# Kernel tuning notes

Measured on AMD Instinct MI355X. Metric: run time of the kernel, lower is better.

## Reference

```python
import jax, jax.numpy as jnp
import numpy as np

NUM_HEADS = 16


def setup_inputs() -> dict:
    key = jax.random.key(0)
    k1, k2, k3 = jax.random.split(key, 3)
    B, N, C = 8, 1024, 1024
    x = jax.random.normal(k1, (B, N, C), dtype=jnp.float32)
    w_qkv = jax.random.normal(k2, (3 * C, C), dtype=jnp.float32) * (C ** -0.5)
    w_proj = jax.random.normal(k3, (C, C), dtype=jnp.float32) * (C ** -0.5)
    b_proj = jnp.zeros((C,), dtype=jnp.float32)
    return {"x": x, "w_qkv": w_qkv, "w_proj": w_proj, "b_proj": b_proj}


def reference(x, w_qkv, w_proj, b_proj):
    B, N, C = x.shape
    H = NUM_HEADS
    d = C // H
    scale = d ** -0.5
    # qkv projection: (B, N, 3C) -> (3, B, H, N, d)
    qkv = jnp.einsum('bnc,oc->bno', x, w_qkv)
    qkv = qkv.reshape(B, N, 3, H, d).transpose(2, 0, 3, 1, 4)
    q, k, v = qkv[0], qkv[1], qkv[2]
    # spatial attention
    attn = jnp.einsum('bhnd,bhmd->bhnm', q, k) * scale
    attn = jax.nn.softmax(attn, axis=-1)
    out = jnp.einsum('bhnm,bhmd->bhnd', attn, v)
    out = out.transpose(0, 2, 1, 3).reshape(B, N, C)
    # output projection
    return jnp.einsum('bnc,oc->bno', out, w_proj) + b_proj
```

## Files before the change

kernel.cpp:

```cpp
#include <hip/hip_runtime.h>
#include <hip/hip_bf16.h>

typedef unsigned short u16;
typedef unsigned int u32;
typedef __bf16 bf16x8 __attribute__((ext_vector_type(8)));
typedef float f32x4 __attribute__((ext_vector_type(4)));

__device__ __forceinline__ u16 f2b(float f) {
    __bf16 h = (__bf16)f;
    return __builtin_bit_cast(u16, h);
}
__device__ __forceinline__ f32x4 mfma16(bf16x8 a, bf16x8 b, f32x4 c) {
    return __builtin_amdgcn_mfma_f32_16x16x32_bf16(a, b, c, 0, 0, 0);
}
__device__ __forceinline__ void async16(const u16* gsrc, u16* ldst) {
    __builtin_amdgcn_global_load_lds(
        (const __attribute__((address_space(1))) void*)gsrc,
        (__attribute__((address_space(3))) void*)ldst, 16, 0, 0);
}

__global__ __launch_bounds__(256) void cvt_f32_bf16(const float* __restrict__ in,
                                                    u16* __restrict__ out, int n) {
    int i = (blockIdx.x * 256 + threadIdx.x) * 4;
    if (i >= n) return;
    float4 f = *(const float4*)(in + i);
    ushort4 o;
    o.x = f2b(f.x); o.y = f2b(f.y); o.z = f2b(f.z); o.w = f2b(f.w);
    *(ushort4*)(out + i) = o;
}

template <bool F32OUT>
__global__ __launch_bounds__(256) void gemm_bt(const u16* __restrict__ A,
                                               const u16* __restrict__ B,
                                               void* __restrict__ Cptr,
                                               const float* __restrict__ bias,
                                               int N, int K) {
    __shared__ u16 As[128 * 32];
    __shared__ u16 Bs[128 * 32];
    const int tid  = threadIdx.x;
    const int lane = tid & 63, wid = tid >> 6;
    const int quad = lane >> 4, l16 = lane & 15;
    const int bm = blockIdx.y, bn = blockIdx.x;
    const int wm = (wid >> 1) * 64, wn = (wid & 1) * 64;
    const int srow = tid >> 2;
    const int scol = (tid & 3) * 8;

    const u16* Abase = A + (size_t)(bm * 128) * K + scol;
    const u16* Bbase = B + (size_t)(bn * 128) * K + scol;

    f32x4 acc[4][4] = {};

    for (int k0 = 0; k0 < K; k0 += 32) {
        __syncthreads();
        async16(Abase + (size_t)srow * K + k0,        &As[wid * 512]);
        async16(Abase + (size_t)(64 + srow) * K + k0, &As[2048 + wid * 512]);
        async16(Bbase + (size_t)srow * K + k0,        &Bs[wid * 512]);
        async16(Bbase + (size_t)(64 + srow) * K + k0, &Bs[2048 + wid * 512]);
        __syncthreads();
        bf16x8 af[4], bfr[4];
#pragma unroll
        for (int mt = 0; mt < 4; mt++)
            af[mt] = *(const bf16x8*)&As[(wm + mt * 16 + l16) * 32 + quad * 8];
#pragma unroll
        for (int nt = 0; nt < 4; nt++)
            bfr[nt] = *(const bf16x8*)&Bs[(wn + nt * 16 + l16) * 32 + quad * 8];
#pragma unroll
        for (int mt = 0; mt < 4; mt++)
#pragma unroll
            for (int nt = 0; nt < 4; nt++)
                acc[mt][nt] = mfma16(af[mt], bfr[nt], acc[mt][nt]);
    }
#pragma unroll
    for (int mt = 0; mt < 4; mt++) {
#pragma unroll
        for (int nt = 0; nt < 4; nt++) {
            int row = bm * 128 + wm + mt * 16 + quad * 4;
            int col = bn * 128 + wn + nt * 16 + l16;
            float bv = F32OUT ? bias[col] : 0.f;
#pragma unroll
            for (int r = 0; r < 4; r++) {
                if (F32OUT)
                    ((float*)Cptr)[(size_t)(row + r) * N + col] = acc[mt][nt][r] + bv;
                else
                    ((u16*)Cptr)[(size_t)(row + r) * N + col] = f2b(acc[mt][nt][r]);
            }
        }
    }
}

__global__ __launch_bounds__(256, 4) void attn_kernel(const u16* __restrict__ qk,
                                                      const u16* __restrict__ vT,
                                                      u16* __restrict__ outb) {
    __shared__ u16 Qs[64 * 64];
    __shared__ u16 Ks[64 * 64];
    __shared__ u16 Vt[64 * 64];
    __shared__ u16 Ps[4 * 16 * 72];
    const int tid = threadIdx.x, lane = tid & 63, wid = tid >> 6;
    const int quad = lane >> 4, l16 = lane & 15;
    const int qt = blockIdx.x;
    const int bh = blockIdx.y;
    const int b = bh >> 4, h = bh & 15;
    const size_t base = (size_t)b * 1024;
    const int hoff = h * 64;
    const float CEXP = 0.125f * 1.44269504f;

    const int sr_ = lane >> 3;
    const int sc_ = ((lane & 7) ^ sr_) * 8;
    const int sw = l16 & 7;

#pragma unroll
    for (int j = 0; j < 2; ++j) {
        int rg = wid * 16 + j * 8;
        async16(qk + (base + qt * 64 + rg + sr_) * 2048 + hoff + sc_, &Qs[rg * 64]);
    }

    f32x4 Oacc[4] = {};
    float l_i[4] = {0.f, 0.f, 0.f, 0.f};
    bf16x8 aq[2];
    u16* Pw = &Ps[wid * (16 * 72)];

    for (int kt = 0; kt < 16; ++kt) {
        __syncthreads();
#pragma unroll
        for (int j = 0; j < 2; ++j) {
            int rg = wid * 16 + j * 8;
            async16(qk + (base + kt * 64 + rg + sr_) * 2048 + 1024 + hoff + sc_,
                    &Ks[rg * 64]);
            async16(vT + (size_t)(hoff + rg + sr_) * 8192 + base + kt * 64 + sc_,
                    &Vt[rg * 64]);
        }
        __syncthreads();

        if (kt == 0) {
            int row = wid * 16 + l16;
            aq[0] = *(const bf16x8*)&Qs[row * 64 + ((quad ^ sw) << 3)];
            aq[1] = *(const bf16x8*)&Qs[row * 64 + (((4 + quad) ^ sw) << 3)];
        }

        f32x4 sacc[4] = {};
#pragma unroll
        for (int nt = 0; nt < 4; nt++) {
            int row = nt * 16 + l16;
            bf16x8 bk0 = *(const bf16x8*)&Ks[row * 64 + ((quad ^ sw) << 3)];
            bf16x8 bk1 = *(const bf16x8*)&Ks[row * 64 + (((4 + quad) ^ sw) << 3)];
            sacc[nt] = mfma16(aq[0], bk0, sacc[nt]);
            sacc[nt] = mfma16(aq[1], bk1, sacc[nt]);
        }

#pragma unroll
        for (int nt = 0; nt < 4; nt++)
#pragma unroll
            for (int r = 0; r < 4; r++) {
                float p = exp2f(sacc[nt][r] * CEXP);
                l_i[r] += p;
                Pw[(quad * 4 + r) * 72 + nt * 16 + l16] = f2b(p);
            }

        asm volatile("s_waitcnt lgkmcnt(0)" ::: "memory");
        __builtin_amdgcn_wave_barrier();

#pragma unroll
        for (int kc = 0; kc < 2; kc++) {
            bf16x8 ap = *(const bf16x8*)&Pw[l16 * 72 + kc * 32 + quad * 8];
#pragma unroll
            for (int nv = 0; nv < 4; nv++) {
                int row = nv * 16 + l16;
                bf16x8 bv = *(const bf16x8*)&Vt[row * 64 + (((kc * 4 + quad) ^ sw) << 3)];
                Oacc[nv] = mfma16(ap, bv, Oacc[nv]);
            }
        }
    }

#pragma unroll
    for (int off = 1; off < 16; off <<= 1)
#pragma unroll
        for (int r = 0; r < 4; r++) l_i[r] += __shfl_xor(l_i[r], off);

    float inv[4];
#pragma unroll
    for (int r = 0; r < 4; r++) inv[r] = 1.f / l_i[r];
#pragma unroll
    for (int nv = 0; nv < 4; nv++)
#pragma unroll
        for (int r = 0; r < 4; r++) {
            int row = qt * 64 + wid * 16 + quad * 4 + r;
            int col = hoff + nv * 16 + l16;
            outb[(base + row) * 1024 + col] = f2b(Oacc[nv][r] * inv[r]);
        }
}

extern "C" void kernel_launch(void* const* d_in, const int* in_sizes, int n_in,
                              void* d_out, int out_size, void* d_ws, size_t ws_size,
                              hipStream_t stream) {
    const float* x      = (const float*)d_in[0];
    const float* w_qkv  = (const float*)d_in[1];
    const float* w_proj = (const float*)d_in[2];
    const float* b_proj = (const float*)d_in[3];

    char* ws = (char*)d_ws;
    u16* xb     = (u16*)(ws);
    u16* wqkvb  = (u16*)(ws + 16777216);
    u16* wprojb = (u16*)(ws + 23068672);
    u16* qkb    = (u16*)(ws + 25165824);
    u16* vTb    = (u16*)(ws + 58720256);
    u16* attnb  = (u16*)(ws + 75497472);

    cvt_f32_bf16<<<8192, 256, 0, stream>>>(x, xb, 8388608);
    cvt_f32_bf16<<<3072, 256, 0, stream>>>(w_qkv, wqkvb, 3145728);
    cvt_f32_bf16<<<1024, 256, 0, stream>>>(w_proj, wprojb, 1048576);

    gemm_bt<false><<<dim3(16, 64), 256, 0, stream>>>(xb, wqkvb, qkb, nullptr, 2048, 1024);
    gemm_bt<false><<<dim3(64, 8), 256, 0, stream>>>(wqkvb + (size_t)2048 * 1024, xb, vTb,
                                                    nullptr, 8192, 1024);
    attn_kernel<<<dim3(16, 128), 256, 0, stream>>>(qkb, vTb, attnb);
    gemm_bt<true><<<dim3(8, 64), 256, 0, stream>>>(attnb, wprojb, d_out, b_proj, 1024, 1024);
}
```

Baseline: 283.3 us.

## Merge conversion and QKV GEMM launches, transpose score MFMA for packed P stores

The three f32-to-bf16 conversion kernels become one launch that picks its source by index, and the QK and V-transposed GEMMs become a single 1536-block launch sharing a common device routine. This removes launch gaps and the tail of each small grid. In the attention kernel the QK^T MFMA swaps its operands so each lane holds four consecutive keys of one query row. P can then be stored as packed 8-byte writes instead of scalar 2-byte stores, and the row-sum reduction uses fewer shuffles. The operand swap changes the accumulator layout, so correctness depends on the new P indexing and the final sum broadcast matching it.

```diff
diff --git a/kernel.cpp b/kernel.cpp
--- a/kernel.cpp
+++ b/kernel.cpp
@@ -10,6 +10,9 @@
     __bf16 h = (__bf16)f;
     return __builtin_bit_cast(u16, h);
 }
+__device__ __forceinline__ u32 f2b2(float lo, float hi) {
+    return (u32)f2b(lo) | ((u32)f2b(hi) << 16);
+}
 __device__ __forceinline__ f32x4 mfma16(bf16x8 a, bf16x8 b, f32x4 c) {
     return __builtin_amdgcn_mfma_f32_16x16x32_bf16(a, b, c, 0, 0, 0);
 }
@@ -19,28 +22,33 @@
         (__attribute__((address_space(3))) void*)ldst, 16, 0, 0);
 }
 
-__global__ __launch_bounds__(256) void cvt_f32_bf16(const float* __restrict__ in,
-                                                    u16* __restrict__ out, int n) {
+__global__ __launch_bounds__(256) void cvt_all(const float* __restrict__ x,
+                                               const float* __restrict__ wq,
+                                               const float* __restrict__ wp,
+                                               u16* __restrict__ xb,
+                                               u16* __restrict__ wqb,
+                                               u16* __restrict__ wpb) {
     int i = (blockIdx.x * 256 + threadIdx.x) * 4;
-    if (i >= n) return;
-    float4 f = *(const float4*)(in + i);
+    const float* src; u16* dst; int off;
+    if (i < 8388608)       { src = x;  dst = xb;  off = i; }
+    else if (i < 11534336) { src = wq; dst = wqb; off = i - 8388608; }
+    else                   { src = wp; dst = wpb; off = i - 11534336; }
+    float4 f = *(const float4*)(src + off);
     ushort4 o;
     o.x = f2b(f.x); o.y = f2b(f.y); o.z = f2b(f.z); o.w = f2b(f.w);
-    *(ushort4*)(out + i) = o;
+    *(ushort4*)(dst + off) = o;
 }
 
 template <bool F32OUT>
-__global__ __launch_bounds__(256) void gemm_bt(const u16* __restrict__ A,
-                                               const u16* __restrict__ B,
-                                               void* __restrict__ Cptr,
-                                               const float* __restrict__ bias,
-                                               int N, int K) {
-    __shared__ u16 As[128 * 32];
-    __shared__ u16 Bs[128 * 32];
+__device__ __forceinline__ void gemm_core(const u16* __restrict__ A,
+                                          const u16* __restrict__ B,
+                                          void* __restrict__ Cptr,
+                                          const float* __restrict__ bias,
+                                          int N, int K, int bm, int bn,
+                                          u16* As, u16* Bs) {
     const int tid  = threadIdx.x;
     const int lane = tid & 63, wid = tid >> 6;
     const int quad = lane >> 4, l16 = lane & 15;
-    const int bm = blockIdx.y, bn = blockIdx.x;
     const int wm = (wid >> 1) * 64, wn = (wid & 1) * 64;
     const int srow = tid >> 2;
     const int scol = (tid & 3) * 8;
@@ -86,6 +94,31 @@
             }
         }
     }
+}
+
+__global__ __launch_bounds__(256) void gemm_qkvt(const u16* __restrict__ xb,
+                                                 const u16* __restrict__ wqkvb,
+                                                 u16* __restrict__ qkb,
+                                                 u16* __restrict__ vTb) {
+    __shared__ u16 As[128 * 32];
+    __shared__ u16 Bs[128 * 32];
+    int id = blockIdx.x;
+    if (id < 1024) {
+        gemm_core<false>(xb, wqkvb, qkb, nullptr, 2048, 1024, id >> 4, id & 15, As, Bs);
+    } else {
+        int t = id - 1024;
+        gemm_core<false>(wqkvb + (size_t)2048 * 1024, xb, vTb, nullptr,
+                         8192, 1024, t >> 6, t & 63, As, Bs);
+    }
+}
+
+__global__ __launch_bounds__(256) void gemm_proj(const u16* __restrict__ A,
+                                                 const u16* __restrict__ B,
+                                                 void* __restrict__ C,
+                                                 const float* __restrict__ bias) {
+    __shared__ u16 As[128 * 32];
+    __shared__ u16 Bs[128 * 32];
+    gemm_core<true>(A, B, C, bias, 1024, 1024, blockIdx.y, blockIdx.x, As, Bs);
 }
 
 __global__ __launch_bounds__(256, 4) void attn_kernel(const u16* __restrict__ qk,
@@ -115,8 +148,8 @@
     }
 
     f32x4 Oacc[4] = {};
-    float l_i[4] = {0.f, 0.f, 0.f, 0.f};
-    bf16x8 aq[2];
+    float lp[4] = {0.f, 0.f, 0.f, 0.f};
+    bf16x8 bq[2];
     u16* Pw = &Ps[wid * (16 * 72)];
 
     for (int kt = 0; kt < 16; ++kt) {
@@ -133,28 +166,30 @@
 
         if (kt == 0) {
             int row = wid * 16 + l16;
-            aq[0] = *(const bf16x8*)&Qs[row * 64 + ((quad ^ sw) << 3)];
-            aq[1] = *(const bf16x8*)&Qs[row * 64 + (((4 + quad) ^ sw) << 3)];
+            bq[0] = *(const bf16x8*)&Qs[row * 64 + ((quad ^ sw) << 3)];
+            bq[1] = *(const bf16x8*)&Qs[row * 64 + (((4 + quad) ^ sw) << 3)];
         }
 
         f32x4 sacc[4] = {};
 #pragma unroll
         for (int nt = 0; nt < 4; nt++) {
             int row = nt * 16 + l16;
-            bf16x8 bk0 = *(const bf16x8*)&Ks[row * 64 + ((quad ^ sw) << 3)];
-            bf16x8 bk1 = *(const bf16x8*)&Ks[row * 64 + (((4 + quad) ^ sw) << 3)];
-            sacc[nt] = mfma16(aq[0], bk0, sacc[nt]);
-            sacc[nt] = mfma16(aq[1], bk1, sacc[nt]);
-        }
-
-#pragma unroll
-        for (int nt = 0; nt < 4; nt++)
-#pragma unroll
-            for (int r = 0; r < 4; r++) {
-                float p = exp2f(sacc[nt][r] * CEXP);
-                l_i[r] += p;
-                Pw[(quad * 4 + r) * 72 + nt * 16 + l16] = f2b(p);
-            }
+            bf16x8 ak0 = *(const bf16x8*)&Ks[row * 64 + ((quad ^ sw) << 3)];
+            bf16x8 ak1 = *(const bf16x8*)&Ks[row * 64 + (((4 + quad) ^ sw) << 3)];
+            sacc[nt] = mfma16(ak0, bq[0], sacc[nt]);
+            sacc[nt] = mfma16(ak1, bq[1], sacc[nt]);
+        }
+
+#pragma unroll
+        for (int nt = 0; nt < 4; nt++) {
+            float p0 = exp2f(sacc[nt][0] * CEXP);
+            float p1 = exp2f(sacc[nt][1] * CEXP);
+            float p2 = exp2f(sacc[nt][2] * CEXP);
+            float p3 = exp2f(sacc[nt][3] * CEXP);
+            lp[0] += p0; lp[1] += p1; lp[2] += p2; lp[3] += p3;
+            uint2 pk; pk.x = f2b2(p0, p1); pk.y = f2b2(p2, p3);
+            *(uint2*)&Pw[l16 * 72 + nt * 16 + quad * 4] = pk;
+        }
 
         asm volatile("s_waitcnt lgkmcnt(0)" ::: "memory");
         __builtin_amdgcn_wave_barrier();
@@ -171,14 +206,13 @@
         }
     }
 
-#pragma unroll
-    for (int off = 1; off < 16; off <<= 1)
-#pragma unroll
-        for (int r = 0; r < 4; r++) l_i[r] += __shfl_xor(l_i[r], off);
-
+    float l = (lp[0] + lp[1]) + (lp[2] + lp[3]);
+    l += __shfl_xor(l, 16);
+    l += __shfl_xor(l, 32);
     float inv[4];
 #pragma unroll
-    for (int r = 0; r < 4; r++) inv[r] = 1.f / l_i[r];
+    for (int r = 0; r < 4; r++) inv[r] = 1.f / __shfl(l, quad * 4 + r);
+
 #pragma unroll
     for (int nv = 0; nv < 4; nv++)
 #pragma unroll
@@ -205,13 +239,8 @@
     u16* vTb    = (u16*)(ws + 58720256);
     u16* attnb  = (u16*)(ws + 75497472);
 
-    cvt_f32_bf16<<<8192, 256, 0, stream>>>(x, xb, 8388608);
-    cvt_f32_bf16<<<3072, 256, 0, stream>>>(w_qkv, wqkvb, 3145728);
-    cvt_f32_bf16<<<1024, 256, 0, stream>>>(w_proj, wprojb, 1048576);
-
-    gemm_bt<false><<<dim3(16, 64), 256, 0, stream>>>(xb, wqkvb, qkb, nullptr, 2048, 1024);
-    gemm_bt<false><<<dim3(64, 8), 256, 0, stream>>>(wqkvb + (size_t)2048 * 1024, xb, vTb,
-                                                    nullptr, 8192, 1024);
+    cvt_all<<<12288, 256, 0, stream>>>(x, w_qkv, w_proj, xb, wqkvb, wprojb);
+    gemm_qkvt<<<1536, 256, 0, stream>>>(xb, wqkvb, qkb, vTb);
     attn_kernel<<<dim3(16, 128), 256, 0, stream>>>(qkb, vTb, attnb);
-    gemm_bt<true><<<dim3(8, 64), 256, 0, stream>>>(attnb, wprojb, d_out, b_proj, 1024, 1024);
-}
+    gemm_proj<<<dim3(8, 64), 256, 0, stream>>>(attnb, wprojb, d_out, b_proj);
+}
```

After: 250.3 us. 1.13x faster.
